# Performance work log

Measured on AMD Instinct MI355X. Metric: run time of the kernel, lower is better.

## Reference

```python
import jax, jax.numpy as jnp
import numpy as np

NEG_FILL = -10000.0  # matches masked_fill_(mask, -10000.0)


def setup_inputs() -> dict:
    key0 = jax.random.key(0)
    kq, kk, kv, km = jax.random.split(key0, 4)
    B, H, S, D = 2, 16, 2048, 64
    query = jax.random.normal(kq, (B, H, S, D), dtype=jnp.float32)
    key = jax.random.normal(kk, (B, H, S, D), dtype=jnp.float32)
    value = jax.random.normal(kv, (B, H, S, D), dtype=jnp.float32)
    # key-padding mask [B, S]; True = position is masked out
    mask = jax.random.randint(km, (B, S), 0, 2).astype(jnp.bool_)
    return {"query": query, "key": key, "value": value, "mask": mask}


def reference(query, key, value, mask):
    # scaled dot-product attention: [B,H,S,D] x [B,H,S,D] -> [B,H,S,S]
    scale = 1.0 / jnp.sqrt(jnp.asarray(query.shape[-1], query.dtype))
    scores = jnp.einsum('bhqd,bhkd->bhqk', query, key) * scale
    # mask [B,S] -> broadcast over heads and query positions as [B,1,1,S]
    scores = jnp.where(mask[:, None, None, :], jnp.asarray(NEG_FILL, scores.dtype), scores)
    attn = jax.nn.softmax(scores, axis=-1)
    # dropout probs are 0 (eval-mode identity)
    out = jnp.einsum('bhqk,bhkd->bhqd', attn, value)
    return out
```

## Files before the change

### kernel.cpp

```cpp
#include <hip/hip_runtime.h>
#include <hip/hip_bf16.h>
#include <stdint.h>

namespace {

constexpr int Bb = 2;
constexpr int Hh = 16;
constexpr int Ss = 2048;
constexpr int Dd = 64;
constexpr int KT = 64;
constexpr int NT = Ss / KT;
constexpr int TILE_BYTES = KT * Dd * 2;
constexpr int BH_BYTES = NT * TILE_BYTES;
constexpr size_t KPRE_BYTES = (size_t)Bb * Hh * Ss * Dd * 2;
constexpr size_t VPRE_OFF = KPRE_BYTES;
constexpr size_t MASK_OFF = 2 * KPRE_BYTES;

typedef __bf16 bf16x8 __attribute__((ext_vector_type(8)));
typedef float floatx4 __attribute__((ext_vector_type(4)));

__global__ __launch_bounds__(256) void preprocess4(
    const float* __restrict__ K, const float* __restrict__ V,
    const int* __restrict__ mask, uint8_t* __restrict__ ws)
{
  const int tid = threadIdx.x;
  const int kt = blockIdx.x;
  const int bh = blockIdx.y;

  if (blockIdx.z == 0) {
    const int c = tid & 7;
#pragma unroll
    for (int half = 0; half < 2; ++half) {
      const int row = (tid >> 3) + half * 32;
      const float4* src = (const float4*)(K + ((size_t)bh * 2048 + kt * 64 + row) * 64 + c * 8);
      const float4 a = src[0], b2 = src[1];
      bf16x8 pk;
      pk[0] = (__bf16)a.x;  pk[1] = (__bf16)a.y;  pk[2] = (__bf16)a.z;  pk[3] = (__bf16)a.w;
      pk[4] = (__bf16)b2.x; pk[5] = (__bf16)b2.y; pk[6] = (__bf16)b2.z; pk[7] = (__bf16)b2.w;
      uint8_t* dst = ws + (size_t)bh * BH_BYTES + kt * TILE_BYTES + row * 128 + ((c ^ (row & 7)) << 4);
      *(bf16x8*)dst = pk;
    }
    if (bh == 0 && kt < 16) {
      const int i = kt * 256 + tid;
      const int bb = i >> 11, key = i & 2047;
      const unsigned long long bal = __ballot(mask[bb * 2048 + key] != 0);
      if ((key & 63) == 0)
        ((unsigned long long*)(ws + MASK_OFF))[bb * NT + (key >> 6)] = bal;
    }
    return;
  }

  const int d2  = tid & 31;
  const int c16 = tid >> 5;
  const int s2 = c16 & 1, q = c16 >> 1;
  const int k0 = 32 * s2 + 4 * q;
  const float* vbase = V + ((size_t)bh * 2048 + kt * 64) * 64;
  float2 col[8];
#pragma unroll
  for (int j = 0; j < 4; ++j) {
    col[j]     = *(const float2*)(vbase + (size_t)(k0 + j) * 64 + 2 * d2);
    col[4 + j] = *(const float2*)(vbase + (size_t)(k0 + 16 + j) * 64 + 2 * d2);
  }
#pragma unroll
  for (int h = 0; h < 2; ++h) {
    const int d = 2 * d2 + h;
    bf16x8 pv;
#pragma unroll
    for (int j = 0; j < 4; ++j) {
      pv[j]     = (__bf16)(h ? col[j].y     : col[j].x);
      pv[4 + j] = (__bf16)(h ? col[4 + j].y : col[4 + j].x);
    }
    uint8_t* dst = ws + VPRE_OFF + (size_t)bh * BH_BYTES + kt * TILE_BYTES + d * 128 + ((c16 ^ (d & 7)) << 4);
    *(bf16x8*)dst = pv;
  }
}

#define NEGM (-14426.950408889634f)
#define MFMA16 __builtin_amdgcn_mfma_f32_16x16x32_bf16

__global__ __launch_bounds__(256, 2) void attn_fused10(
    const float* __restrict__ Q, const uint8_t* __restrict__ ws,
    float* __restrict__ Out)
{
  const int tid  = threadIdx.x;
  const int wave = tid >> 6;
  const int lane = tid & 63;
  const int ln   = lane & 15;
  const int quad = lane >> 4;

  const int bh   = blockIdx.x;
  const int qblk = blockIdx.y;
  const int b    = bh >> 4;

  const float* Qb = Q + (size_t)bh * Ss * Dd;
  float*       Ob = Out + (size_t)bh * Ss * Dd;
  const uint8_t* Kpre = ws + (size_t)bh * BH_BYTES;
  const uint8_t* Vpre = ws + VPRE_OFF + (size_t)bh * BH_BYTES;
  const unsigned long long* Mbits = (const unsigned long long*)(ws + MASK_OFF) + b * NT;

  const int q0A = qblk * 128 + wave * 32;
  const int q0B = q0A + 16;

  const float QS = 0.125f * 1.44269504088896340736f;
  bf16x8 aqA0, aqA1, aqB0, aqB1;
  {
    const float* qpA = Qb + (size_t)(q0A + ln) * Dd + quad * 8;
    const float* qpB = Qb + (size_t)(q0B + ln) * Dd + quad * 8;
#pragma unroll
    for (int j = 0; j < 8; ++j) {
      aqA0[j] = (__bf16)(qpA[j] * QS);
      aqA1[j] = (__bf16)(qpA[32 + j] * QS);
      aqB0[j] = (__bf16)(qpB[j] * QS);
      aqB1[j] = (__bf16)(qpB[32 + j] * QS);
    }
  }

  floatx4 oA[4], oB[4];
  floatx4 laccA = (floatx4){0.f, 0.f, 0.f, 0.f};
  floatx4 laccB = (floatx4){0.f, 0.f, 0.f, 0.f};
#pragma unroll
  for (int nd = 0; nd < 4; ++nd) {
    oA[nd] = (floatx4){0.f, 0.f, 0.f, 0.f};
    oB[nd] = (floatx4){0.f, 0.f, 0.f, 0.f};
  }

  const int swz0 = (quad ^ (ln & 7)) << 4;
  const int swz1 = ((quad + 4) ^ (ln & 7)) << 4;
  const int vsw0 = ((quad * 2 + 0) ^ (ln & 7)) << 4;
  const int vsw1 = ((quad * 2 + 1) ^ (ln & 7)) << 4;

  auto loadK = [&](const uint8_t* Kb, int sub, bf16x8& b0, bf16x8& b1) {
    const uint8_t* krow = Kb + (sub * 16 + ln) * 128;
    b0 = *(const bf16x8*)(krow + swz0);
    b1 = *(const bf16x8*)(krow + swz1);
  };
  auto loadV = [&](const uint8_t* Vb, int s2, bf16x8* w) {
    const int vsw = s2 ? vsw1 : vsw0;
#pragma unroll
    for (int nd = 0; nd < 4; ++nd)
      w[nd] = *(const bf16x8*)(Vb + (nd * 16 + ln) * 128 + vsw);
  };

  bf16x8 kf0[2][2], kf1[2][2];
  bf16x8 vf[2][4];
  loadK(Kpre, 0, kf0[0][0], kf1[0][0]);
  loadK(Kpre, 1, kf0[0][1], kf1[0][1]);
  loadV(Vpre, 0, vf[0]);

  for (int it = 0; it < NT; ++it) {
    const uint8_t* Kb = Kpre + it * TILE_BYTES;
    const uint8_t* Vb = Vpre + it * TILE_BYTES;
    const unsigned long long mb = Mbits[it];

#pragma unroll
    for (int p = 0; p < 2; ++p) {
      if (p == 0) {
        loadK(Kb, 2, kf0[1][0], kf1[1][0]);
        loadK(Kb, 3, kf0[1][1], kf1[1][1]);
        loadV(Vb, 1, vf[1]);
      } else if (it + 1 < NT) {
        loadK(Kb + TILE_BYTES, 0, kf0[0][0], kf1[0][0]);
        loadK(Kb + TILE_BYTES, 1, kf0[0][1], kf1[0][1]);
        loadV(Vb + TILE_BYTES, 0, vf[0]);
      }

      const uint32_t bits0 = (uint32_t)(mb >> ((2 * p) * 16 + quad * 4));
      const uint32_t bits1 = (uint32_t)(mb >> ((2 * p + 1) * 16 + quad * 4));
      floatx4 sA0, sA1, sB0, sB1;
#pragma unroll
      for (int r = 0; r < 4; ++r) {
        const float b0v = ((bits0 >> r) & 1) ? NEGM : 0.f;
        const float b1v = ((bits1 >> r) & 1) ? NEGM : 0.f;
        sA0[r] = b0v; sB0[r] = b0v;
        sA1[r] = b1v; sB1[r] = b1v;
      }

      __builtin_amdgcn_s_setprio(1);

      sA0 = MFMA16(kf0[p][0], aqA0, sA0, 0, 0, 0);
      sA0 = MFMA16(kf1[p][0], aqA1, sA0, 0, 0, 0);
      sB0 = MFMA16(kf0[p][0], aqB0, sB0, 0, 0, 0);
      sB0 = MFMA16(kf1[p][0], aqB1, sB0, 0, 0, 0);
      sA1 = MFMA16(kf0[p][1], aqA0, sA1, 0, 0, 0);
      sA1 = MFMA16(kf1[p][1], aqA1, sA1, 0, 0, 0);
      sB1 = MFMA16(kf0[p][1], aqB0, sB1, 0, 0, 0);
      sB1 = MFMA16(kf1[p][1], aqB1, sB1, 0, 0, 0);

      bf16x8 bpA, bpB;
#pragma unroll
      for (int r = 0; r < 4; ++r) {
        const float pA0 = __builtin_amdgcn_exp2f(sA0[r]);
        const float pA1 = __builtin_amdgcn_exp2f(sA1[r]);
        const float pB0 = __builtin_amdgcn_exp2f(sB0[r]);
        const float pB1 = __builtin_amdgcn_exp2f(sB1[r]);
        laccA[r] += pA0 + pA1;
        laccB[r] += pB0 + pB1;
        bpA[r] = (__bf16)pA0; bpA[4 + r] = (__bf16)pA1;
        bpB[r] = (__bf16)pB0; bpB[4 + r] = (__bf16)pB1;
      }

#pragma unroll
      for (int nd = 0; nd < 4; ++nd) {
        oA[nd] = MFMA16(vf[p][nd], bpA, oA[nd], 0, 0, 0);
        oB[nd] = MFMA16(vf[p][nd], bpB, oB[nd], 0, 0, 0);
      }
      __builtin_amdgcn_s_setprio(0);
    }
  }

  float lA = (laccA[0] + laccA[1]) + (laccA[2] + laccA[3]);
  float lB = (laccB[0] + laccB[1]) + (laccB[2] + laccB[3]);
  lA += __shfl_xor(lA, 16); lA += __shfl_xor(lA, 32);
  lB += __shfl_xor(lB, 16); lB += __shfl_xor(lB, 32);
  const float iA = 1.0f / lA, iB = 1.0f / lB;
#pragma unroll
  for (int nd = 0; nd < 4; ++nd) {
    float4 wv;
    wv.x = oA[nd][0] * iA; wv.y = oA[nd][1] * iA;
    wv.z = oA[nd][2] * iA; wv.w = oA[nd][3] * iA;
    *(float4*)(Ob + (size_t)(q0A + ln) * Dd + nd * 16 + quad * 4) = wv;
    wv.x = oB[nd][0] * iB; wv.y = oB[nd][1] * iB;
    wv.z = oB[nd][2] * iB; wv.w = oB[nd][3] * iB;
    *(float4*)(Ob + (size_t)(q0B + ln) * Dd + nd * 16 + quad * 4) = wv;
  }
}

}

extern "C" void kernel_launch(void* const* d_in, const int* in_sizes, int n_in,
                              void* d_out, int out_size, void* d_ws, size_t ws_size,
                              hipStream_t stream) {
  const float* Q   = (const float*)d_in[0];
  const float* K   = (const float*)d_in[1];
  const float* V   = (const float*)d_in[2];
  const int*  mask = (const int*)d_in[3];
  float* Out = (float*)d_out;

  preprocess4<<<dim3(32, 32, 2), 256, 0, stream>>>(K, V, mask, (uint8_t*)d_ws);
  attn_fused10<<<dim3(Bb * Hh, Ss / 128), 256, 0, stream>>>(Q, (const uint8_t*)d_ws, Out);
  (void)ws_size; (void)in_sizes; (void)n_in; (void)out_size;
}
```

Before: 146.0 us.

## Stage K/V tiles into LDS via async global_load_lds with triple buffering

K and V tiles are no longer loaded from global memory straight into registers by each wave. All four waves now cooperatively copy them into a three-slot LDS ring buffer with direct global-to-LDS loads, one barrier per tile. The loop is also software-pipelined so the QK^T/softmax phase of tile i overlaps the PV phase of tile i-1. This removes four-fold redundant global reads per block and hides load latency, at the cost of 48KB of LDS, which can limit occupancy, and one __syncthreads per iteration.

New measurement: 139.6 us. 1.05x faster.

```diff
diff --git a/kernel.cpp b/kernel.cpp
--- a/kernel.cpp
+++ b/kernel.cpp
@@ -19,6 +19,13 @@
 typedef __bf16 bf16x8 __attribute__((ext_vector_type(8)));
 typedef float floatx4 __attribute__((ext_vector_type(4)));
 
+typedef __attribute__((address_space(1))) const unsigned int guint;
+typedef __attribute__((address_space(3))) unsigned int luint;
+
+__device__ __forceinline__ void g2lds16(const void* g, void* l) {
+  __builtin_amdgcn_global_load_lds((guint*)g, (luint*)l, 16, 0, 0);
+}
+
 __global__ __launch_bounds__(256) void preprocess4(
     const float* __restrict__ K, const float* __restrict__ V,
     const int* __restrict__ mask, uint8_t* __restrict__ ws)
@@ -78,7 +85,7 @@
 #define NEGM (-14426.950408889634f)
 #define MFMA16 __builtin_amdgcn_mfma_f32_16x16x32_bf16
 
-__global__ __launch_bounds__(256, 2) void attn_fused10(
+__global__ __launch_bounds__(256, 2) void attn_fused11(
     const float* __restrict__ Q, const uint8_t* __restrict__ ws,
     float* __restrict__ Out)
 {
@@ -98,6 +105,9 @@
   const uint8_t* Vpre = ws + VPRE_OFF + (size_t)bh * BH_BYTES;
   const unsigned long long* Mbits = (const unsigned long long*)(ws + MASK_OFF) + b * NT;
 
+  __shared__ __align__(16) __bf16 Klds[3][64 * Dd];
+  __shared__ __align__(16) __bf16 Vlds[3][64 * Dd];
+
   const int q0A = qblk * 128 + wave * 32;
   const int q0B = q0A + 16;
 
@@ -126,87 +136,119 @@
 
   const int swz0 = (quad ^ (ln & 7)) << 4;
   const int swz1 = ((quad + 4) ^ (ln & 7)) << 4;
-  const int vsw0 = ((quad * 2 + 0) ^ (ln & 7)) << 4;
-  const int vsw1 = ((quad * 2 + 1) ^ (ln & 7)) << 4;
-
-  auto loadK = [&](const uint8_t* Kb, int sub, bf16x8& b0, bf16x8& b1) {
-    const uint8_t* krow = Kb + (sub * 16 + ln) * 128;
-    b0 = *(const bf16x8*)(krow + swz0);
-    b1 = *(const bf16x8*)(krow + swz1);
+  const int soff = wave * 1024 + lane * 16;
+
+  auto stage = [&](int it, __bf16* kl_, __bf16* vl_) {
+    const uint8_t* kg = Kpre + it * TILE_BYTES;
+    const uint8_t* vg = Vpre + it * TILE_BYTES;
+    uint8_t* kl = (uint8_t*)kl_;
+    uint8_t* vl = (uint8_t*)vl_;
+    g2lds16(kg + soff,        kl + soff);
+    g2lds16(kg + soff + 4096, kl + soff + 4096);
+    g2lds16(vg + soff,        vl + soff);
+    g2lds16(vg + soff + 4096, vl + soff + 4096);
   };
-  auto loadV = [&](const uint8_t* Vb, int s2, bf16x8* w) {
-    const int vsw = s2 ? vsw1 : vsw0;
-#pragma unroll
-    for (int nd = 0; nd < 4; ++nd)
-      w[nd] = *(const bf16x8*)(Vb + (nd * 16 + ln) * 128 + vsw);
-  };
-
-  bf16x8 kf0[2][2], kf1[2][2];
-  bf16x8 vf[2][4];
-  loadK(Kpre, 0, kf0[0][0], kf1[0][0]);
-  loadK(Kpre, 1, kf0[0][1], kf1[0][1]);
-  loadV(Vpre, 0, vf[0]);
-
-  for (int it = 0; it < NT; ++it) {
-    const uint8_t* Kb = Kpre + it * TILE_BYTES;
-    const uint8_t* Vb = Vpre + it * TILE_BYTES;
-    const unsigned long long mb = Mbits[it];
-
-#pragma unroll
-    for (int p = 0; p < 2; ++p) {
-      if (p == 0) {
-        loadK(Kb, 2, kf0[1][0], kf1[1][0]);
-        loadK(Kb, 3, kf0[1][1], kf1[1][1]);
-        loadV(Vb, 1, vf[1]);
-      } else if (it + 1 < NT) {
-        loadK(Kb + TILE_BYTES, 0, kf0[0][0], kf1[0][0]);
-        loadK(Kb + TILE_BYTES, 1, kf0[0][1], kf1[0][1]);
-        loadV(Vb + TILE_BYTES, 0, vf[0]);
-      }
-
-      const uint32_t bits0 = (uint32_t)(mb >> ((2 * p) * 16 + quad * 4));
-      const uint32_t bits1 = (uint32_t)(mb >> ((2 * p + 1) * 16 + quad * 4));
-      floatx4 sA0, sA1, sB0, sB1;
-#pragma unroll
-      for (int r = 0; r < 4; ++r) {
-        const float b0v = ((bits0 >> r) & 1) ? NEGM : 0.f;
-        const float b1v = ((bits1 >> r) & 1) ? NEGM : 0.f;
-        sA0[r] = b0v; sB0[r] = b0v;
-        sA1[r] = b1v; sB1[r] = b1v;
-      }
-
-      __builtin_amdgcn_s_setprio(1);
-
-      sA0 = MFMA16(kf0[p][0], aqA0, sA0, 0, 0, 0);
-      sA0 = MFMA16(kf1[p][0], aqA1, sA0, 0, 0, 0);
-      sB0 = MFMA16(kf0[p][0], aqB0, sB0, 0, 0, 0);
-      sB0 = MFMA16(kf1[p][0], aqB1, sB0, 0, 0, 0);
-      sA1 = MFMA16(kf0[p][1], aqA0, sA1, 0, 0, 0);
-      sA1 = MFMA16(kf1[p][1], aqA1, sA1, 0, 0, 0);
-      sB1 = MFMA16(kf0[p][1], aqB0, sB1, 0, 0, 0);
-      sB1 = MFMA16(kf1[p][1], aqB1, sB1, 0, 0, 0);
-
-      bf16x8 bpA, bpB;
-#pragma unroll
-      for (int r = 0; r < 4; ++r) {
-        const float pA0 = __builtin_amdgcn_exp2f(sA0[r]);
-        const float pA1 = __builtin_amdgcn_exp2f(sA1[r]);
-        const float pB0 = __builtin_amdgcn_exp2f(sB0[r]);
-        const float pB1 = __builtin_amdgcn_exp2f(sB1[r]);
-        laccA[r] += pA0 + pA1;
-        laccB[r] += pB0 + pB1;
-        bpA[r] = (__bf16)pA0; bpA[4 + r] = (__bf16)pA1;
-        bpB[r] = (__bf16)pB0; bpB[4 + r] = (__bf16)pB1;
-      }
-
-#pragma unroll
-      for (int nd = 0; nd < 4; ++nd) {
-        oA[nd] = MFMA16(vf[p][nd], bpA, oA[nd], 0, 0, 0);
-        oB[nd] = MFMA16(vf[p][nd], bpB, oB[nd], 0, 0, 0);
-      }
-      __builtin_amdgcn_s_setprio(0);
-    }
-  }
+
+#define SPHASE(KB, MB, BPA, BPB)                                              \
+  {                                                                           \
+    const uint8_t* Kb_ = (const uint8_t*)(KB);                                \
+    _Pragma("unroll")                                                         \
+    for (int p = 0; p < 2; ++p) {                                             \
+      const uint8_t* kr0 = Kb_ + ((2 * p) * 16 + ln) * 128;                   \
+      const uint8_t* kr1 = Kb_ + ((2 * p + 1) * 16 + ln) * 128;               \
+      const bf16x8 k00 = *(const bf16x8*)(kr0 + swz0);                        \
+      const bf16x8 k10 = *(const bf16x8*)(kr0 + swz1);                        \
+      const bf16x8 k01 = *(const bf16x8*)(kr1 + swz0);                        \
+      const bf16x8 k11 = *(const bf16x8*)(kr1 + swz1);                        \
+      const uint32_t bits0 = (uint32_t)((MB) >> ((2 * p) * 16 + quad * 4));   \
+      const uint32_t bits1 = (uint32_t)((MB) >> ((2 * p + 1) * 16 + quad * 4));\
+      floatx4 sA0, sA1, sB0, sB1;                                             \
+      _Pragma("unroll")                                                       \
+      for (int r = 0; r < 4; ++r) {                                           \
+        const float b0v = ((bits0 >> r) & 1) ? NEGM : 0.f;                    \
+        const float b1v = ((bits1 >> r) & 1) ? NEGM : 0.f;                    \
+        sA0[r] = b0v; sB0[r] = b0v;                                           \
+        sA1[r] = b1v; sB1[r] = b1v;                                           \
+      }                                                                       \
+      sA0 = MFMA16(k00, aqA0, sA0, 0, 0, 0);                                  \
+      sA0 = MFMA16(k10, aqA1, sA0, 0, 0, 0);                                  \
+      sB0 = MFMA16(k00, aqB0, sB0, 0, 0, 0);                                  \
+      sB0 = MFMA16(k10, aqB1, sB0, 0, 0, 0);                                  \
+      sA1 = MFMA16(k01, aqA0, sA1, 0, 0, 0);                                  \
+      sA1 = MFMA16(k11, aqA1, sA1, 0, 0, 0);                                  \
+      sB1 = MFMA16(k01, aqB0, sB1, 0, 0, 0);                                  \
+      sB1 = MFMA16(k11, aqB1, sB1, 0, 0, 0);                                  \
+      _Pragma("unroll")                                                       \
+      for (int r = 0; r < 4; ++r) {                                           \
+        const float pA0 = __builtin_amdgcn_exp2f(sA0[r]);                     \
+        const float pA1 = __builtin_amdgcn_exp2f(sA1[r]);                     \
+        const float pB0 = __builtin_amdgcn_exp2f(sB0[r]);                     \
+        const float pB1 = __builtin_amdgcn_exp2f(sB1[r]);                     \
+        laccA[r] += pA0 + pA1;                                                \
+        laccB[r] += pB0 + pB1;                                                \
+        BPA[p][r] = (__bf16)pA0; BPA[p][4 + r] = (__bf16)pA1;                 \
+        BPB[p][r] = (__bf16)pB0; BPB[p][4 + r] = (__bf16)pB1;                 \
+      }                                                                       \
+    }                                                                         \
+  }
+
+#define PVPHASE(VB, BPA, BPB)                                                 \
+  {                                                                           \
+    const uint8_t* Vb_ = (const uint8_t*)(VB);                                \
+    _Pragma("unroll")                                                         \
+    for (int p = 0; p < 2; ++p) {                                             \
+      _Pragma("unroll")                                                       \
+      for (int nd = 0; nd < 4; ++nd) {                                        \
+        const uint8_t* vrow = Vb_ + (nd * 16 + ln) * 128;                     \
+        const bf16x8 w =                                                      \
+            *(const bf16x8*)(vrow + (((quad * 2 + p) ^ (ln & 7)) << 4));      \
+        oA[nd] = MFMA16(w, BPA[p], oA[nd], 0, 0, 0);                          \
+        oB[nd] = MFMA16(w, BPB[p], oB[nd], 0, 0, 0);                          \
+      }                                                                       \
+    }                                                                         \
+  }
+
+#define BODY(IT, PBA, PBB, CBA, CBB)                                          \
+  {                                                                           \
+    __syncthreads();                                                          \
+    if ((IT) + 1 < NT) stage((IT) + 1, knext, vnext);                         \
+    const unsigned long long mb_ = Mbits[(IT)];                               \
+    __builtin_amdgcn_s_setprio(1);                                            \
+    SPHASE(kcur, mb_, CBA, CBB);                                              \
+    PVPHASE(vprev, PBA, PBB);                                                 \
+    __builtin_amdgcn_s_setprio(0);                                            \
+    __bf16* t_;                                                               \
+    t_ = kprev; kprev = kcur; kcur = knext; knext = t_;                       \
+    t_ = vprev; vprev = vcur; vcur = vnext; vnext = t_;                       \
+  }
+
+  __bf16 *kprev = Klds[0], *kcur = Klds[1], *knext = Klds[2];
+  __bf16 *vprev = Vlds[0], *vcur = Vlds[1], *vnext = Vlds[2];
+
+  bf16x8 bpA0[2], bpB0[2], bpA1[2], bpB1[2];
+
+  stage(0, kprev, vprev);
+  __syncthreads();
+  stage(1, kcur, vcur);
+  {
+    const unsigned long long mb_ = Mbits[0];
+    __builtin_amdgcn_s_setprio(1);
+    SPHASE(kprev, mb_, bpA0, bpB0);
+    __builtin_amdgcn_s_setprio(0);
+  }
+
+  for (int it = 1; it < 31; it += 2) {
+    BODY(it,     bpA0, bpB0, bpA1, bpB1);
+    BODY(it + 1, bpA1, bpB1, bpA0, bpB0);
+  }
+  BODY(31, bpA0, bpB0, bpA1, bpB1);
+  __builtin_amdgcn_s_setprio(1);
+  PVPHASE(vprev, bpA1, bpB1);
+  __builtin_amdgcn_s_setprio(0);
+
+#undef BODY
+#undef PVPHASE
+#undef SPHASE
 
   float lA = (laccA[0] + laccA[1]) + (laccA[2] + laccA[3]);
   float lB = (laccB[0] + laccB[1]) + (laccB[2] + laccB[3]);
@@ -237,6 +279,6 @@
   float* Out = (float*)d_out;
 
   preprocess4<<<dim3(32, 32, 2), 256, 0, stream>>>(K, V, mask, (uint8_t*)d_ws);
-  attn_fused10<<<dim3(Bb * Hh, Ss / 128), 256, 0, stream>>>(Q, (const uint8_t*)d_ws, Out);
+  attn_fused11<<<dim3(Bb * Hh, Ss / 128), 256, 0, stream>>>(Q, (const uint8_t*)d_ws, Out);
   (void)ws_size; (void)in_sizes; (void)n_in; (void)out_size;
 }
```
